# Optimization experiments

Hardware: AMD Instinct MI355X
Metric: run time of the kernel (lower is better)

Reference implementation:

```python
import jax, jax.numpy as jnp
import numpy as np


def _knn(coords, k):
    # coords: [N, 3]. Returns indices of the k nearest neighbors (self excluded): [N, k]
    sq = jnp.sum(coords * coords, axis=1)
    d2 = sq[:, None] + sq[None, :] - 2.0 * (coords @ coords.T)  # [N, N]
    n = coords.shape[0]
    d2 = jnp.where(jnp.eye(n, dtype=bool), jnp.inf, d2)  # loop=False: no self edges
    _, idx = jax.lax.top_k(-d2, k)
    return idx


def setup_inputs() -> dict:
    key = jax.random.key(0)
    ks = jax.random.split(key, 7)
    B, N, C = 8, 4096, 6
    feats = jax.random.normal(ks[0], (B, N, C), dtype=jnp.float32)
    # Glorot-ish scaled weights; PyG GCNConv lin has no bias, bias added post-aggregation.
    W1 = jax.random.normal(ks[1], (6, 64), dtype=jnp.float32) * (1.0 / np.sqrt(6))
    b1 = jnp.zeros((64,), dtype=jnp.float32)
    W2 = jax.random.normal(ks[2], (64, 128), dtype=jnp.float32) * (1.0 / np.sqrt(64))
    b2 = jnp.zeros((128,), dtype=jnp.float32)
    Wf = jax.random.normal(ks[3], (128, 128), dtype=jnp.float32) * (1.0 / np.sqrt(128))
    bf = jnp.zeros((128,), dtype=jnp.float32)
    return {"feats": feats, "W1": W1, "b1": b1, "W2": W2, "b2": b2,
            "Wf": Wf, "bf": bf, "k": 16}


def reference(feats, W1, b1, W2, b2, Wf, bf, k):
    # feats: [B, N, C]; coords = first 3 channels.
    coords = feats[..., :3]
    nbr = jax.vmap(lambda c: _knn(c, k))(coords)  # [B, N, k]
    inv_deg = 1.0 / (k + 1)  # every node has exactly k in-edges + self loop (uniform sym norm)
    x = feats
    for W, b in ((W1, b1), (W2, b2)):
        h = x @ W  # [B, N, H]
        nb = jax.vmap(lambda hb, ib: hb[ib])(h, nbr)  # gather neighbor feats: [B, N, k, H]
        x = jax.nn.relu((nb.sum(axis=2) + h) * inv_deg + b)  # GCN aggregate + bias + ReLU
    return x @ Wf + bf  # [B, N, out_dim]
```

## Files before the change

### kernel.cpp

```cpp
#include <hip/hip_runtime.h>
#include <cstdint>
#include <cstddef>

#define NPTS 4096
#define KNN  16
#define INV_DEG (1.0f / 17.0f)
#define CAP  48
#define TS   512

typedef unsigned long long u64;
typedef unsigned int u32;
typedef float v2f __attribute__((ext_vector_type(2)));

#define UNUSED_K 0x7F800000FFFFFFFFull
#define SELF_K   0x7F800000FFFFFFFEull

__device__ __forceinline__ double as_f64(u64 k) { return __longlong_as_double((long long)k); }

__global__ __launch_bounds__(512) void knn_kernel(const float* __restrict__ feats,
                                                  const float* __restrict__ W1,
                                                  const float* __restrict__ b1,
                                                  int* __restrict__ nbr,
                                                  float* __restrict__ x1) {
#pragma clang fp contract(off)
  __shared__ float4 sc[TS];
  __shared__ u64 sbuf[8][2][64];

  const int b = blockIdx.x >> 8;
  const int pbase = (blockIdx.x & 255) * 16;
  const float* fb = feats + (size_t)b * NPTS * 6;
  const int wave = threadIdx.x >> 6;
  const int lane = threadIdx.x & 63;

  int ip[2];
  float xi[2], yi[2], zi[2], sqi[2], tau[2];
  u64 slot[2];
  int cnt[2];
#pragma unroll
  for (int p = 0; p < 2; ++p) {
    ip[p] = pbase + wave * 2 + p;
    const float* fr = fb + (size_t)ip[p] * 6;
    xi[p] = fr[0]; yi[p] = fr[1]; zi[p] = fr[2];
    sqi[p] = __fadd_rn(__fadd_rn(__fmul_rn(xi[p], xi[p]), __fmul_rn(yi[p], yi[p])),
                       __fmul_rn(zi[p], zi[p]));
    tau[p] = __uint_as_float(0x7f800000u);
    slot[p] = UNUSED_K;
    cnt[p] = 0;
  }

  auto flush = [&](int p) {
    u64* wb = &sbuf[wave][p][0];
    if (lane >= cnt[p] && lane < CAP) wb[lane] = UNUSED_K;
    if (lane < KNN) wb[CAP + lane] = slot[p];
    u64 myk = wb[lane];
    if ((u32)myk == (u32)ip[p]) {
      myk = SELF_K;
      wb[lane] = SELF_K;
    }
    const double dm = as_f64(myk);
    int rank = 0;
#pragma unroll
    for (int m = 0; m < 64; m += 4) {
      const double k0 = as_f64(wb[m]), k1 = as_f64(wb[m + 1]);
      const double k2 = as_f64(wb[m + 2]), k3 = as_f64(wb[m + 3]);
      rank += (int)(k0 < dm) + (int)(k1 < dm) + (int)(k2 < dm) + (int)(k3 < dm);
    }
    if (rank < KNN) wb[rank] = myk;
    u64 s15 = wb[15];
    if (lane < KNN) slot[p] = wb[lane];
    tau[p] = __uint_as_float((u32)(s15 >> 32));
    cnt[p] = 0;
  };

  for (int tb = 0; tb < NPTS; tb += TS) {
    __syncthreads();
    for (int t = threadIdx.x; t < TS; t += 512) {
      const float* fr = fb + (size_t)(tb + t) * 6;
      const float x = fr[0], y = fr[1], z = fr[2];
      const float sq = __fadd_rn(__fadd_rn(__fmul_rn(x, x), __fmul_rn(y, y)),
                                 __fmul_rn(z, z));
      float4 c; c.x = x; c.y = y; c.z = z; c.w = sq;
      sc[t] = c;
    }
    __syncthreads();

    for (int jb0 = 0; jb0 < TS; jb0 += 64) {
      const int tl = jb0 + lane;
      const int j = tb + tl;
      const float4 c = sc[tl];
      const v2f cx2 = {c.x, c.x}, cy2 = {c.y, c.y}, cz2 = {c.z, c.z},
                sq2 = {c.w, c.w};
      v2f X = {xi[0], xi[1]};
      v2f Y = {yi[0], yi[1]};
      v2f Z = {zi[0], zi[1]};
      v2f SQ = {sqi[0], sqi[1]};
      v2f dot = X * cx2;
      dot = __builtin_elementwise_fma(Y, cy2, dot);
      dot = __builtin_elementwise_fma(Z, cz2, dot);
      v2f two = {2.0f, 2.0f};
      v2f d2v = (SQ + sq2) - two * dot;
      float d2s[2] = {d2v.x, d2v.y};
#pragma unroll
      for (int p = 0; p < 2; ++p) {
        const bool pred = d2s[p] <= tau[p];
        const u64 bal = __ballot(pred);
        if (bal) {
          const int npass = __popcll(bal);
          if (cnt[p] + npass > CAP) flush(p);
          const int pos = cnt[p] + (int)__builtin_amdgcn_mbcnt_hi(
                                        (u32)(bal >> 32),
                                        __builtin_amdgcn_mbcnt_lo((u32)bal, 0));
          const u64 key = ((u64)__float_as_uint(d2s[p]) << 32) | (u32)j;
          if (npass <= CAP) {
            if (pred) sbuf[wave][p][pos] = key;
            cnt[p] += npass;
          } else {
            if (pred && pos < CAP) sbuf[wave][p][pos] = key;
            cnt[p] = CAP;
            flush(p);
            if (pred && pos >= CAP) sbuf[wave][p][pos - CAP] = key;
            cnt[p] = npass - CAP;
          }
        }
      }
    }
  }
#pragma unroll
  for (int p = 0; p < 2; ++p) flush(p);

  float* fsc = (float*)&sbuf[wave][0][0];
  float w1r[6];
#pragma unroll
  for (int k = 0; k < 6; ++k) w1r[k] = W1[k * 64 + lane];
  const float b1r = b1[lane];

#pragma unroll
  for (int p = 0; p < 2; ++p) {
    const int n = b * NPTS + ip[p];
    const int row = (lane < KNN) ? (int)(u32)slot[p] : ip[p];
    if (lane < KNN)
      nbr[(size_t)n * KNN + lane] = row;
    if (lane < 17) {
      const float* fr = fb + (size_t)row * 6;
      float2 r0 = *(const float2*)(fr);
      float2 r1 = *(const float2*)(fr + 2);
      float2 r2 = *(const float2*)(fr + 4);
      fsc[lane * 6 + 0] = r0.x; fsc[lane * 6 + 1] = r0.y;
      fsc[lane * 6 + 2] = r1.x; fsc[lane * 6 + 3] = r1.y;
      fsc[lane * 6 + 4] = r2.x; fsc[lane * 6 + 5] = r2.y;
    }
    __syncthreads();
    if (lane < 6) {
      float s = 0.f;
#pragma unroll
      for (int t = 0; t < 17; ++t) s += fsc[t * 6 + lane];
      fsc[102 + lane] = s;
    }
    __syncthreads();
    float s = 0.f;
#pragma unroll
    for (int k = 0; k < 6; ++k) s = fmaf(fsc[102 + k], w1r[k], s);
    x1[(size_t)n * 64 + lane] = fmaxf(fmaf(s, INV_DEG, b1r), 0.f);
    __syncthreads();
  }
}

__global__ __launch_bounds__(256) void enc23_kernel(const float* __restrict__ x1,
                                                    const int* __restrict__ nbr,
                                                    const float* __restrict__ W2,
                                                    const float* __restrict__ b2,
                                                    const float* __restrict__ Wf,
                                                    const float* __restrict__ bf,
                                                    float* __restrict__ out) {
  __shared__ float a1s[16][64];
  __shared__ v2f wt[16][64];
  __shared__ float xs[16][128];
  const int tid = threadIdx.x;
  const int n0 = blockIdx.x * 16;
  const int gb = n0 & ~(NPTS - 1);
  const int wave = tid >> 6, lane = tid & 63;

  {
    const int p = tid >> 4, c4 = tid & 15;
    const int n = n0 + p;
    const int* nb = nbr + (size_t)n * KNN;
    float4 s = ((const float4*)(x1 + (size_t)n * 64))[c4];
#pragma unroll
    for (int t = 0; t < KNN; ++t) {
      float4 v = ((const float4*)(x1 + (size_t)(gb + nb[t]) * 64))[c4];
      s.x += v.x; s.y += v.y; s.z += v.z; s.w += v.w;
    }
    *((float4*)&a1s[p][c4 * 4]) = s;
  }

  const int p0 = wave * 4;
  const float bx = b2[lane], by = b2[lane + 64];

  v2f acc[4];
#pragma unroll
  for (int i = 0; i < 4; ++i) acc[i] = (v2f){0, 0};
  for (int kt = 0; kt < 64; kt += 16) {
    __syncthreads();
#pragma unroll
    for (int i = 0; i < 4; ++i) {
      const int e = tid + 256 * i;
      const int k = e >> 6, l = e & 63;
      v2f w;
      w.x = W2[(kt + k) * 128 + l];
      w.y = W2[(kt + k) * 128 + 64 + l];
      wt[k][l] = w;
    }
    __syncthreads();
    for (int kk = 0; kk < 16; kk += 4) {
      float4 a[4];
#pragma unroll
      for (int i = 0; i < 4; ++i) a[i] = *(const float4*)&a1s[p0 + i][kt + kk];
#pragma unroll
      for (int j = 0; j < 4; ++j) {
        const v2f w = wt[kk + j][lane];
#pragma unroll
        for (int i = 0; i < 4; ++i) {
          const float e = j == 0 ? a[i].x : j == 1 ? a[i].y : j == 2 ? a[i].z
                                                                     : a[i].w;
          v2f v = {e, e};
          acc[i] = __builtin_elementwise_fma(v, w, acc[i]);
        }
      }
    }
  }
#pragma unroll
  for (int pi = 0; pi < 4; ++pi) {
    xs[p0 + pi][lane] = fmaxf(fmaf(acc[pi].x, INV_DEG, bx), 0.f);
    xs[p0 + pi][lane + 64] = fmaxf(fmaf(acc[pi].y, INV_DEG, by), 0.f);
  }

  v2f facc[4];
#pragma unroll
  for (int i = 0; i < 4; ++i) facc[i] = (v2f){0, 0};
  for (int jt = 0; jt < 128; jt += 16) {
    __syncthreads();
#pragma unroll
    for (int i = 0; i < 4; ++i) {
      const int e = tid + 256 * i;
      const int j = e >> 6, l = e & 63;
      v2f w;
      w.x = Wf[(jt + j) * 128 + l];
      w.y = Wf[(jt + j) * 128 + 64 + l];
      wt[j][l] = w;
    }
    __syncthreads();
    for (int jj = 0; jj < 16; jj += 4) {
      float4 a[4];
#pragma unroll
      for (int i = 0; i < 4; ++i) a[i] = *(const float4*)&xs[p0 + i][jt + jj];
#pragma unroll
      for (int j2 = 0; j2 < 4; ++j2) {
        const v2f w = wt[jj + j2][lane];
#pragma unroll
        for (int i = 0; i < 4; ++i) {
          const float e = j2 == 0 ? a[i].x : j2 == 1 ? a[i].y : j2 == 2 ? a[i].z
                                                                        : a[i].w;
          v2f v = {e, e};
          facc[i] = __builtin_elementwise_fma(v, w, facc[i]);
        }
      }
    }
  }
  const float fx = bf[lane], fy = bf[lane + 64];
#pragma unroll
  for (int pi = 0; pi < 4; ++pi) {
    float* row = out + (size_t)(n0 + p0 + pi) * 128;
    row[lane] = facc[pi].x + fx;
    row[lane + 64] = facc[pi].y + fy;
  }
}

extern "C" void kernel_launch(void* const* d_in, const int* in_sizes, int n_in,
                              void* d_out, int out_size, void* d_ws, size_t ws_size,
                              hipStream_t stream) {
  const float* feats = (const float*)d_in[0];
  const float* W1 = (const float*)d_in[1];
  const float* b1 = (const float*)d_in[2];
  const float* W2 = (const float*)d_in[3];
  const float* b2 = (const float*)d_in[4];
  const float* Wf = (const float*)d_in[5];
  const float* bf = (const float*)d_in[6];
  float* out = (float*)d_out;

  char* ws = (char*)d_ws;
  int* nbr = (int*)ws;
  float* x1 = (float*)(ws + (size_t)(2 << 20));

  knn_kernel<<<2048, 512, 0, stream>>>(feats, W1, b1, nbr, x1);
  enc23_kernel<<<2048, 256, 0, stream>>>(x1, nbr, W2, b2, Wf, bf, out);
}
```

Measured before the change: 229.7 us.

## Double-buffer weight tiles and process 32 points per block in enc23

```diff
diff --git a/kernel.cpp b/kernel.cpp
--- a/kernel.cpp
+++ b/kernel.cpp
@@ -172,54 +172,72 @@
                                                     const float* __restrict__ Wf,
                                                     const float* __restrict__ bf,
                                                     float* __restrict__ out) {
-  __shared__ float a1s[16][64];
-  __shared__ v2f wt[16][64];
-  __shared__ float xs[16][128];
+  __shared__ float a1s[32][64];
+  __shared__ v2f wt[2][16][64];
+  __shared__ float xs[32][128];
   const int tid = threadIdx.x;
-  const int n0 = blockIdx.x * 16;
+  const int n0 = blockIdx.x * 32;
   const int gb = n0 & ~(NPTS - 1);
   const int wave = tid >> 6, lane = tid & 63;
 
   {
-    const int p = tid >> 4, c4 = tid & 15;
-    const int n = n0 + p;
-    const int* nb = nbr + (size_t)n * KNN;
-    float4 s = ((const float4*)(x1 + (size_t)n * 64))[c4];
-#pragma unroll
-    for (int t = 0; t < KNN; ++t) {
-      float4 v = ((const float4*)(x1 + (size_t)(gb + nb[t]) * 64))[c4];
-      s.x += v.x; s.y += v.y; s.z += v.z; s.w += v.w;
-    }
-    *((float4*)&a1s[p][c4 * 4]) = s;
-  }
-
-  const int p0 = wave * 4;
+    const int c4 = tid & 15;
+#pragma unroll
+    for (int pass = 0; pass < 2; ++pass) {
+      const int p = (tid >> 4) + pass * 16;
+      const int n = n0 + p;
+      const int* nb = nbr + (size_t)n * KNN;
+      float4 s = ((const float4*)(x1 + (size_t)n * 64))[c4];
+#pragma unroll
+      for (int t = 0; t < KNN; ++t) {
+        float4 v = ((const float4*)(x1 + (size_t)(gb + nb[t]) * 64))[c4];
+        s.x += v.x; s.y += v.y; s.z += v.z; s.w += v.w;
+      }
+      *((float4*)&a1s[p][c4 * 4]) = s;
+    }
+  }
+
+  const int p0 = wave * 8;
   const float bx = b2[lane], by = b2[lane + 64];
 
-  v2f acc[4];
-#pragma unroll
-  for (int i = 0; i < 4; ++i) acc[i] = (v2f){0, 0};
-  for (int kt = 0; kt < 64; kt += 16) {
-    __syncthreads();
+  v2f wreg[4];
+  auto loadW = [&](const float* __restrict__ W, int kt) {
 #pragma unroll
     for (int i = 0; i < 4; ++i) {
       const int e = tid + 256 * i;
       const int k = e >> 6, l = e & 63;
-      v2f w;
-      w.x = W2[(kt + k) * 128 + l];
-      w.y = W2[(kt + k) * 128 + 64 + l];
-      wt[k][l] = w;
-    }
-    __syncthreads();
+      wreg[i].x = W[(kt + k) * 128 + l];
+      wreg[i].y = W[(kt + k) * 128 + 64 + l];
+    }
+  };
+  auto storeW = [&](int buf) {
+#pragma unroll
+    for (int i = 0; i < 4; ++i) {
+      const int e = tid + 256 * i;
+      wt[buf][e >> 6][e & 63] = wreg[i];
+    }
+  };
+
+  loadW(W2, 0);
+  storeW(0);
+  __syncthreads();
+
+  v2f acc[8];
+#pragma unroll
+  for (int i = 0; i < 8; ++i) acc[i] = (v2f){0, 0};
+  for (int kt_i = 0; kt_i < 4; ++kt_i) {
+    if (kt_i < 3) loadW(W2, (kt_i + 1) * 16);
+    const int cur = kt_i & 1;
+    const int kt = kt_i * 16;
     for (int kk = 0; kk < 16; kk += 4) {
-      float4 a[4];
-#pragma unroll
-      for (int i = 0; i < 4; ++i) a[i] = *(const float4*)&a1s[p0 + i][kt + kk];
+      float4 a[8];
+#pragma unroll
+      for (int i = 0; i < 8; ++i) a[i] = *(const float4*)&a1s[p0 + i][kt + kk];
 #pragma unroll
       for (int j = 0; j < 4; ++j) {
-        const v2f w = wt[kk + j][lane];
-#pragma unroll
-        for (int i = 0; i < 4; ++i) {
+        const v2f w = wt[cur][kk + j][lane];
+#pragma unroll
+        for (int i = 0; i < 8; ++i) {
           const float e = j == 0 ? a[i].x : j == 1 ? a[i].y : j == 2 ? a[i].z
                                                                      : a[i].w;
           v2f v = {e, e};
@@ -227,37 +245,35 @@
         }
       }
     }
-  }
-#pragma unroll
-  for (int pi = 0; pi < 4; ++pi) {
+    if (kt_i < 3) storeW(cur ^ 1);
+    __syncthreads();
+  }
+#pragma unroll
+  for (int pi = 0; pi < 8; ++pi) {
     xs[p0 + pi][lane] = fmaxf(fmaf(acc[pi].x, INV_DEG, bx), 0.f);
     xs[p0 + pi][lane + 64] = fmaxf(fmaf(acc[pi].y, INV_DEG, by), 0.f);
   }
 
-  v2f facc[4];
-#pragma unroll
-  for (int i = 0; i < 4; ++i) facc[i] = (v2f){0, 0};
-  for (int jt = 0; jt < 128; jt += 16) {
-    __syncthreads();
-#pragma unroll
-    for (int i = 0; i < 4; ++i) {
-      const int e = tid + 256 * i;
-      const int j = e >> 6, l = e & 63;
-      v2f w;
-      w.x = Wf[(jt + j) * 128 + l];
-      w.y = Wf[(jt + j) * 128 + 64 + l];
-      wt[j][l] = w;
-    }
-    __syncthreads();
+  loadW(Wf, 0);
+  storeW(0);
+  __syncthreads();
+
+  v2f facc[8];
+#pragma unroll
+  for (int i = 0; i < 8; ++i) facc[i] = (v2f){0, 0};
+  for (int jt_i = 0; jt_i < 8; ++jt_i) {
+    if (jt_i < 7) loadW(Wf, (jt_i + 1) * 16);
+    const int cur = jt_i & 1;
+    const int jt = jt_i * 16;
     for (int jj = 0; jj < 16; jj += 4) {
-      float4 a[4];
-#pragma unroll
-      for (int i = 0; i < 4; ++i) a[i] = *(const float4*)&xs[p0 + i][jt + jj];
+      float4 a[8];
+#pragma unroll
+      for (int i = 0; i < 8; ++i) a[i] = *(const float4*)&xs[p0 + i][jt + jj];
 #pragma unroll
       for (int j2 = 0; j2 < 4; ++j2) {
-        const v2f w = wt[jj + j2][lane];
-#pragma unroll
-        for (int i = 0; i < 4; ++i) {
+        const v2f w = wt[cur][jj + j2][lane];
+#pragma unroll
+        for (int i = 0; i < 8; ++i) {
           const float e = j2 == 0 ? a[i].x : j2 == 1 ? a[i].y : j2 == 2 ? a[i].z
                                                                         : a[i].w;
           v2f v = {e, e};
@@ -265,10 +281,12 @@
         }
       }
     }
+    if (jt_i < 7) storeW(cur ^ 1);
+    __syncthreads();
   }
   const float fx = bf[lane], fy = bf[lane + 64];
 #pragma unroll
-  for (int pi = 0; pi < 4; ++pi) {
+  for (int pi = 0; pi < 8; ++pi) {
     float* row = out + (size_t)(n0 + p0 + pi) * 128;
     row[lane] = facc[pi].x + fx;
     row[lane + 64] = facc[pi].y + fy;
@@ -292,5 +310,5 @@
   float* x1 = (float*)(ws + (size_t)(2 << 20));
 
   knn_kernel<<<2048, 512, 0, stream>>>(feats, W1, b1, nbr, x1);
-  enc23_kernel<<<2048, 256, 0, stream>>>(x1, nbr, W2, b2, Wf, bf, out);
+  enc23_kernel<<<1024, 256, 0, stream>>>(x1, nbr, W2, b2, Wf, bf, out);
 }
```

Result: slower. 245.1 us (+6.7%).
